# Kernel optimization log

Measured on AMD Instinct MI355X. Metric: run time of the kernel, lower is better.

Reference implementation:

```python
import jax, jax.numpy as jnp
import numpy as np
import math

B, P, D_MODEL, H = 4, 900, 512, 8
NSHOT = 1
SIGMA = 5.0


def setup_inputs() -> dict:
    key = jax.random.key(0)
    ks = jax.random.split(key, 9)
    d, h = D_MODEL, H
    return {
        "query": jax.random.normal(ks[0], (B, P, d), jnp.float32),
        "key_t": jax.random.normal(ks[1], (NSHOT * B, P, d), jnp.float32),
        "value": jax.random.uniform(ks[2], (B, NSHOT * P), dtype=jnp.float32),
        "Wq": jax.random.normal(ks[3], (d, d), jnp.float32) * 0.02,
        "bq": jnp.zeros((d,), jnp.float32),
        "Wk": jax.random.normal(ks[4], (d, d), jnp.float32) * 0.02,
        "bk": jnp.zeros((d,), jnp.float32),
        "conv1_w": jax.random.normal(ks[5], (4 * h, h, 3, 3), jnp.float32) * 0.05,
        "conv1_b": jnp.zeros((4 * h,), jnp.float32),
        "conv2_w": jax.random.normal(ks[6], (h, 4 * h, 3, 3), jnp.float32) * 0.05,
        "conv2_b": jnp.zeros((h,), jnp.float32),
        "nshot": NSHOT,
    }


def _apply_gaussian_kernel(corr, sigma=SIGMA):
    # corr: [Bn, head, HW, W] with HW == W and W a perfect square
    Bn, head, HW, W = corr.shape
    BH = Bn * head
    side = int(round(math.sqrt(W)))
    c = corr.reshape(BH, HW, side, side)
    idx = jnp.argmax(c, axis=1)                                  # [BH, side, side]
    idx_y = (idx // side).astype(jnp.float32)[:, None, None, :, :]
    idx_x = (idx % side).astype(jnp.float32)[:, None, None, :, :]
    xs = jnp.linspace(-1.0, 1.0, side).reshape(1, 1, side, 1, 1)
    ys = jnp.linspace(-1.0, 1.0, side).reshape(1, side, 1, 1, 1)
    # NOTE: original code compares linspace coords to raw integer argmax coords
    gauss = jnp.exp(-((xs - idx_x) ** 2 + (ys - idx_y) ** 2) / (2.0 * sigma ** 2))
    gauss = gauss.reshape(BH, HW, side, side)                    # [BH, h0*w0, h1, w1]
    return (gauss * c).reshape(Bn, head, HW, W)


def reference(query, key_t, value, Wq, bq, Wk, bk, conv1_w, conv1_b, conv2_w, conv2_b, nshot):
    h = conv2_w.shape[0]
    d_model = Wq.shape[0]
    dk = d_model // h
    b, p, _ = query.shape
    n = int(nshot)

    q = (query @ Wq.T + bq).reshape(b, p, h, dk).transpose(0, 2, 1, 3)          # [b,h,p,dk]
    k = (key_t @ Wk.T + bk).reshape(n, b, p, h, dk)
    k = k.transpose(1, 3, 0, 2, 4).reshape(b, h, n * p, dk)                     # [b,h,np,dk]

    scores = jnp.einsum('bhpc,bhqc->bhpq', q, k)                                 # [b,h,p,n*p]

    # gaussian modulation: 'b head h (n w) -> (b n) head h w'
    s = scores.reshape(b, h, p, n, p).transpose(0, 3, 1, 2, 4).reshape(b * n, h, p, p)
    s = _apply_gaussian_kernel(s)
    scores = s.reshape(b, n, h, p, p).transpose(0, 2, 3, 1, 4).reshape(b, h, p, n * p)

    scores = scores / math.sqrt(dk)
    attn = jax.nn.softmax(scores, axis=-1)                                       # [b,h,p,np]

    def conv(x, w, bias):
        y = jax.lax.conv_general_dilated(x, w, (1, 1), 'SAME',
                                         dimension_numbers=('NCHW', 'OIHW', 'NCHW'))
        return jax.nn.relu(y + bias[None, :, None, None])

    attn = conv(attn, conv1_w, conv1_b)
    attn = conv(attn, conv2_w, conv2_b)

    x = jnp.einsum('bhpq,bq->bhp', attn, value)[..., None]                        # [b,h,p,1]
    return jnp.mean(x, axis=1)                                                    # [b,p,1]
```

## Files before the change

kernel.cpp:

```cpp
#include <hip/hip_runtime.h>

#define NB 4
#define NP 900
#define ND 512
#define NH 8
#define NDK 64
#define NROWS (NB*NP)
#define SSZ (NP*NP)
#define NBH (NB*NH)
#define SIDE 30

typedef unsigned short ushort_t;
typedef unsigned char uchar_t;
typedef unsigned long long u64_t;
typedef __attribute__((ext_vector_type(8)))  _Float16 h8v;
typedef __attribute__((ext_vector_type(4)))  float  f4v;
typedef __attribute__((ext_vector_type(16))) float  f16v;

__device__ __forceinline__ ushort_t f2h(float f) {
    union { _Float16 h; ushort_t u; } c; c.h = (_Float16)f; return c.u;
}
__device__ __forceinline__ float h2f(ushort_t u) {
    union { _Float16 h; ushort_t u; } c; c.u = u; return (float)c.h;
}
__device__ __forceinline__ unsigned int fenc(float v) {
    unsigned int b = __float_as_uint(v);
    return (b & 0x80000000u) ? ~b : (b | 0x80000000u);
}

__global__ __launch_bounds__(256) void proj_kernel(
    const float* __restrict__ query, const float* __restrict__ key_t,
    const float* __restrict__ Wq, const float* __restrict__ bq,
    const float* __restrict__ Wk, const float* __restrict__ bk,
    float* __restrict__ Qo, float* __restrict__ Ko, u64_t* __restrict__ amax)
{
    const float *X, *W, *bias;
    float* O;
    if (blockIdx.z == 0) { X = query; W = Wq; bias = bq; O = Qo; }
    else                 { X = key_t; W = Wk; bias = bk; O = Ko; }

    if (blockIdx.z == 0) {
        const int t = (blockIdx.y * 57 + blockIdx.x) * 256 + threadIdx.x;
        if (t < NBH * NP) amax[t] = 0ull;
    }

    __shared__ __align__(16) float As[16][68];
    __shared__ __align__(16) float Bs[16][68];

    const int i0 = blockIdx.x * 64;
    const int h  = blockIdx.y;
    const int j0 = h * 64;
    const int tid = threadIdx.x;
    const int tx = tid & 15, ty = tid >> 4;

    float acc[4][4] = {};

    for (int k0 = 0; k0 < ND; k0 += 16) {
        const int r  = tid >> 2;
        const int kk = (tid & 3) * 4;
        float4 av = make_float4(0.f, 0.f, 0.f, 0.f);
        const int gi = i0 + r;
        if (gi < NROWS) av = *(const float4*)(X + (size_t)gi * ND + k0 + kk);
        As[kk+0][r] = av.x; As[kk+1][r] = av.y; As[kk+2][r] = av.z; As[kk+3][r] = av.w;
        const float4 bv = *(const float4*)(W + (size_t)(j0 + r) * ND + k0 + kk);
        Bs[kk+0][r] = bv.x; Bs[kk+1][r] = bv.y; Bs[kk+2][r] = bv.z; Bs[kk+3][r] = bv.w;
        __syncthreads();
        #pragma unroll
        for (int k = 0; k < 16; ++k) {
            const float4 a4 = *(const float4*)&As[k][ty*4];
            const float4 b4 = *(const float4*)&Bs[k][tx*4];
            const float aa[4] = {a4.x, a4.y, a4.z, a4.w};
            const float bb[4] = {b4.x, b4.y, b4.z, b4.w};
            #pragma unroll
            for (int ii = 0; ii < 4; ++ii)
                #pragma unroll
                for (int jj = 0; jj < 4; ++jj)
                    acc[ii][jj] = fmaf(aa[ii], bb[jj], acc[ii][jj]);
        }
        __syncthreads();
    }

    #pragma unroll
    for (int ii = 0; ii < 4; ++ii) {
        const int gi = i0 + ty*4 + ii;
        if (gi >= NROWS) continue;
        const int b = gi / NP, p = gi - b * NP;
        float4 o;
        o.x = acc[ii][0] + bias[j0 + tx*4 + 0];
        o.y = acc[ii][1] + bias[j0 + tx*4 + 1];
        o.z = acc[ii][2] + bias[j0 + tx*4 + 2];
        o.w = acc[ii][3] + bias[j0 + tx*4 + 3];
        *(float4*)(O + ((size_t)(b*NH + h)*NP + p)*NDK + tx*4) = o;
    }
}

__global__ __launch_bounds__(256, 2) void scores_kernel(
    const float* __restrict__ Q, const float* __restrict__ K, ushort_t* __restrict__ Sh,
    u64_t* __restrict__ amax)
{
    __shared__ __align__(16) ushort_t Qs[128][128];
    __shared__ __align__(16) ushort_t Ks[128][128];
    __shared__ u64_t amax_s[128];

    const int lin = blockIdx.x;
    const int swz = (lin & 7) * 256 + (lin >> 3);
    const int bh  = swz >> 6;
    const int p0  = ((swz >> 3) & 7) * 128;
    const int q0  = (swz & 7) * 128;

    const float* Qb = Q + (size_t)bh * NP * NDK;
    const float* Kb = K + (size_t)bh * NP * NDK;
    const int tid  = threadIdx.x;
    const int lane = tid & 63;
    const int w    = tid >> 6;

    if (tid < 128) amax_s[tid] = 0ull;

    #pragma unroll
    for (int i = 0; i < 8; ++i) {
        const int idx = tid + i * 256;
        const int r = idx >> 4, c4 = idx & 15;
        float4 qv = make_float4(0.f,0.f,0.f,0.f);
        float4 kv = make_float4(0.f,0.f,0.f,0.f);
        if (p0 + r < NP) qv = *(const float4*)(Qb + (size_t)(p0 + r) * NDK + c4*4);
        if (q0 + r < NP) kv = *(const float4*)(Kb + (size_t)(q0 + r) * NDK + c4*4);
        const int ch  = (c4 >> 1) ^ (r & 7);
        const int off = (c4 & 1) * 8;
        const float qf[4] = {qv.x, qv.y, qv.z, qv.w};
        const float kf[4] = {kv.x, kv.y, kv.z, kv.w};
        ushort_t qh[4], ql[4], kh[4], kl[4];
        #pragma unroll
        for (int j = 0; j < 4; ++j) {
            qh[j] = f2h(qf[j]); ql[j] = f2h(qf[j] - h2f(qh[j]));
            kh[j] = f2h(kf[j]); kl[j] = f2h(kf[j] - h2f(kh[j]));
        }
        char* qrow = (char*)&Qs[r][0];
        char* krow = (char*)&Ks[r][0];
        uint2 u;
        u.x = (unsigned)qh[0] | ((unsigned)qh[1] << 16);
        u.y = (unsigned)qh[2] | ((unsigned)qh[3] << 16);
        *(uint2*)(qrow + ch*16 + off) = u;
        u.x = (unsigned)ql[0] | ((unsigned)ql[1] << 16);
        u.y = (unsigned)ql[2] | ((unsigned)ql[3] << 16);
        *(uint2*)(qrow + (ch + 8)*16 + off) = u;
        u.x = (unsigned)kh[0] | ((unsigned)kh[1] << 16);
        u.y = (unsigned)kh[2] | ((unsigned)kh[3] << 16);
        *(uint2*)(krow + ch*16 + off) = u;
        u.x = (unsigned)kl[0] | ((unsigned)kl[1] << 16);
        u.y = (unsigned)kl[2] | ((unsigned)kl[3] << 16);
        *(uint2*)(krow + (ch + 8)*16 + off) = u;
    }
    __syncthreads();

    const int ln = lane & 31;
    const int lh = lane >> 5;
    const int wr = (w >> 1) * 64;
    const int wc = (w & 1) * 64;

    auto ldQ = [&](int row, int ch) -> h8v {
        return *(const h8v*)((const char*)&Qs[row][0] + ((ch ^ (row & 7)) << 4));
    };
    auto ldK = [&](int row, int ch) -> h8v {
        return *(const h8v*)((const char*)&Ks[row][0] + ((ch ^ (row & 7)) << 4));
    };

    f16v acc[2][2] = {};

    #pragma unroll
    for (int ks = 0; ks < 4; ++ks) {
        const int chH = ks*2 + lh;
        h8v ah[2], al[2], bhv[2], blv[2];
        #pragma unroll
        for (int t = 0; t < 2; ++t) {
            const int row = wr + t*32 + ln;
            const int col = wc + t*32 + ln;
            ah[t]  = ldQ(row, chH);
            al[t]  = ldQ(row, chH + 8);
            bhv[t] = ldK(col, chH);
            blv[t] = ldK(col, chH + 8);
        }
        #pragma unroll
        for (int rb = 0; rb < 2; ++rb)
            #pragma unroll
            for (int cb = 0; cb < 2; ++cb) {
                acc[rb][cb] = __builtin_amdgcn_mfma_f32_32x32x16_f16(ah[rb], bhv[cb], acc[rb][cb], 0, 0, 0);
                acc[rb][cb] = __builtin_amdgcn_mfma_f32_32x32x16_f16(ah[rb], blv[cb], acc[rb][cb], 0, 0, 0);
                acc[rb][cb] = __builtin_amdgcn_mfma_f32_32x32x16_f16(al[rb], bhv[cb], acc[rb][cb], 0, 0, 0);
            }
    }

    ushort_t* Sb = Sh + (size_t)bh * SSZ;
    #pragma unroll
    for (int rb = 0; rb < 2; ++rb) {
        #pragma unroll
        for (int cb = 0; cb < 2; ++cb) {
            const int lq = wc + cb*32 + ln;
            const int gq = q0 + lq;
            if (gq < NP) {
                u64_t key = 0ull;
                #pragma unroll
                for (int r = 0; r < 16; ++r) {
                    const int gp = p0 + wr + rb*32 + ((r & 3) + 8*(r >> 2) + 4*lh);
                    if (gp < NP) {
                        const float v = acc[rb][cb][r];
                        Sb[(size_t)gp * NP + gq] = f2h(v);
                        const u64_t kk = ((u64_t)fenc(v) << 32) | (unsigned)(899 - gp);
                        key = key > kk ? key : kk;
                    }
                }
                atomicMax(&amax_s[lq], key);
            }
        }
    }
    __syncthreads();
    if (tid < 128 && q0 + tid < NP)
        atomicMax(&amax[(size_t)bh * NP + q0 + tid], amax_s[tid]);
}

__global__ __launch_bounds__(256) void decode_kernel(
    const u64_t* __restrict__ amax, uchar_t* __restrict__ gidx)
{
    const int t = blockIdx.x * 256 + threadIdx.x;
    if (t >= NBH * NP) return;
    const int idx = 899 - (int)(unsigned)(amax[t] & 0xFFFFFFFFull);
    gidx[2*t]   = (uchar_t)(idx % SIDE);
    gidx[2*t+1] = (uchar_t)(idx / SIDE);
}

__global__ __launch_bounds__(256) void modulate_softmax_kernel(
    const ushort_t* __restrict__ S, const uchar_t* __restrict__ gidx, ushort_t* __restrict__ S2,
    float* __restrict__ out)
{
    __shared__ __align__(16) ushort_t ob[NP][NH];
    __shared__ float TX[SIDE], TY[SIDE];

    const int p = blockIdx.x;
    const int b = blockIdx.y;
    const int tid = threadIdx.x;
    const int lane = tid & 63;
    const int w = tid >> 6;

    if (p == 0)
        for (int q = tid; q < NP; q += 256) out[(size_t)b*NP + q] = 0.f;

    const float ax = -1.f + (2.f/29.f) * (float)(p % SIDE);
    const float ay = -1.f + (2.f/29.f) * (float)(p / SIDE);

    if (tid < SIDE) {
        const float d = ax - (float)tid;
        TX[tid] = __expf(-d*d * 0.02f);
    } else if (tid >= 64 && tid < 64 + SIDE) {
        const int j = tid - 64;
        const float d = ay - (float)j;
        TY[j] = __expf(-d*d * 0.02f);
    }
    __syncthreads();

    #pragma unroll 1
    for (int hh = 0; hh < 2; ++hh) {
        const int h = w + hh*4;
        const ushort_t* row = S + (size_t)(b*NH + h)*SSZ + (size_t)p*NP;
        const uchar_t* gp = gidx + (size_t)(b*NH + h)*NP*2;

        float rv[16];
        float lmax = -3.4e38f;
        #pragma unroll
        for (int i = 0; i < 8; ++i) {
            const int q2 = 2*lane + 128*i;
            float v0 = -3.4e38f, v1 = -3.4e38f;
            if (q2 < NP) {
                const unsigned u = *(const unsigned*)(row + q2);
                const uchar4 g4 = *(const uchar4*)(gp + 2*q2);
                v0 = h2f((ushort_t)(u & 0xFFFFu)) * TX[g4.x] * TY[g4.y] * 0.125f;
                v1 = h2f((ushort_t)(u >> 16))     * TX[g4.z] * TY[g4.w] * 0.125f;
            }
            rv[2*i]   = v0;
            rv[2*i+1] = v1;
            lmax = fmaxf(lmax, fmaxf(v0, v1));
        }
        #pragma unroll
        for (int off = 32; off > 0; off >>= 1)
            lmax = fmaxf(lmax, __shfl_xor(lmax, off, 64));

        float lsum = 0.f;
        #pragma unroll
        for (int i = 0; i < 16; ++i) {
            const int q = 2*lane + 128*(i >> 1) + (i & 1);
            const float e = (q < NP) ? __expf(rv[i] - lmax) : 0.f;
            rv[i] = e;
            lsum += e;
        }
        #pragma unroll
        for (int off = 32; off > 0; off >>= 1)
            lsum += __shfl_xor(lsum, off, 64);
        const float inv = 1.f / lsum;

        #pragma unroll
        for (int i = 0; i < 8; ++i) {
            const int q2 = 2*lane + 128*i;
            if (q2 < NP) {
                ob[q2][h]   = f2h(rv[2*i]   * inv);
                ob[q2+1][h] = f2h(rv[2*i+1] * inv);
            }
        }
    }
    __syncthreads();
    for (int q = tid; q < NP; q += 256)
        *(uint4*)(S2 + (((size_t)b*NP + p)*NP + q)*NH) = *(const uint4*)&ob[q][0];
}

__global__ void prep_weights_kernel(
    const float* __restrict__ c1w, const float* __restrict__ c2w,
    ushort_t* __restrict__ w1b, ushort_t* __restrict__ w2b)
{
    const int tid = threadIdx.x;
    for (int i = tid; i < 5*64; i += 256) {
        const int c = i >> 6, l = i & 63;
        const int oc = l & 31, hf = l >> 5;
        #pragma unroll
        for (int j = 0; j < 8; ++j) {
            float wv;
            if (c < 4)      wv = c1w[(oc*8 + j)*9 + (2*c + hf)];
            else            wv = hf ? 0.f : c1w[(oc*8 + j)*9 + 8];
            w1b[(i)*8 + j] = f2h(wv);
        }
    }
    for (int i = tid; i < 9*64; i += 256) {
        const int t = i >> 6, l = i & 63;
        const int n = l & 15, qd = l >> 4;
        #pragma unroll
        for (int j = 0; j < 8; ++j) {
            const int k = qd*8 + j;
            const float wv = (n < 8) ? c2w[(n*32 + k)*9 + t] : 0.f;
            w2b[(i)*8 + j] = f2h(wv);
        }
    }
}

__global__ __launch_bounds__(256, 4) void conv_mfma_kernel(
    const ushort_t* __restrict__ S2, const ushort_t* __restrict__ w1b,
    const ushort_t* __restrict__ w2b,
    const float* __restrict__ b1, const float* __restrict__ b2,
    const float* __restrict__ value, float* __restrict__ out)
{
    __shared__ __align__(16) ushort_t a_s[4][13][34][8];
    __shared__ __align__(16) ushort_t c1row[4][34][40];

    const int tid  = threadIdx.x;
    const int lane = tid & 63;
    const int w    = tid >> 6;
    const int b    = blockIdx.z;
    const int gx0  = blockIdx.x * 30;
    const int gy0w = blockIdx.y * 36 + w * 9;

    c1row[w][32 + (lane >> 5)][lane & 31] = 0;

    for (int i = lane; i < 13*34; i += 64) {
        const int ai = i / 34, xi = i - ai*34;
        const int gp = gy0w - 2 + ai, gq = gx0 - 2 + xi;
        uint4 v = make_uint4(0u,0u,0u,0u);
        if ((unsigned)gp < (unsigned)NP && (unsigned)gq < (unsigned)NP)
            v = *(const uint4*)(S2 + (((size_t)b*NP + gp)*NP + gq)*NH);
        *(uint4*)&a_s[w][ai][xi][0] = v;
    }

    h8v w1f[5], w2f[9];
    #pragma unroll
    for (int c = 0; c < 5; ++c) w1f[c] = *(const h8v*)(w1b + ((size_t)c*64 + lane)*8);
    #pragma unroll
    for (int t = 0; t < 9; ++t) w2f[t] = *(const h8v*)(w2b + ((size_t)t*64 + lane)*8);

    const float b1v = b1[lane & 31];
    const float b2v = ((lane & 15) < 8) ? b2[lane & 15] : 0.f;

    const int m    = lane & 31;
    const int half = lane >> 5;
    const int m16  = lane & 15;
    const int qd   = lane >> 4;

    float vseg[2][4];
    #pragma unroll
    for (int g = 0; g < 2; ++g)
        #pragma unroll
        for (int r = 0; r < 4; ++r) {
            const int ql = g*16 + qd*4 + r;
            vseg[g][r] = (ql < 30) ? value[b*NP + gx0 + ql] : 0.f;
        }

    auto lda = [&](int y, int x) -> h8v {
        return *(const h8v*)&a_s[w][y][x][0];
    };

    f4v o0[3] = {}, o1[3] = {};

    #pragma unroll
    for (int yc = 0; yc < 11; ++yc) {
        {
            const bool rowok = (unsigned)(gy0w - 1 + yc) < (unsigned)NP;
            const h8v A0 = lda(yc,        m + half);
            const h8v A1 = lda(yc + half, half ? m : (m + 2));
            const h8v A2 = lda(yc + 1,    m + 1 + half);
            const h8v A3 = lda(yc + 2,    m + half);
            const h8v A4 = lda(yc + 2,    m + 2);
            f16v acc = {};
            acc = __builtin_amdgcn_mfma_f32_32x32x16_f16(A0, w1f[0], acc, 0, 0, 0);
            acc = __builtin_amdgcn_mfma_f32_32x32x16_f16(A1, w1f[1], acc, 0, 0, 0);
            acc = __builtin_amdgcn_mfma_f32_32x32x16_f16(A2, w1f[2], acc, 0, 0, 0);
            acc = __builtin_amdgcn_mfma_f32_32x32x16_f16(A3, w1f[3], acc, 0, 0, 0);
            acc = __builtin_amdgcn_mfma_f32_32x32x16_f16(A4, w1f[4], acc, 0, 0, 0);
            #pragma unroll
            for (int r = 0; r < 16; ++r) {
                const int x_l = (r & 3) + 8*(r >> 2) + 4*half;
                float f = fmaxf(acc[r] + b1v, 0.f);
                const bool ok = rowok && ((unsigned)(gx0 - 1 + x_l) < (unsigned)NP);
                f = ok ? f : 0.f;
                c1row[w][x_l][lane & 31] = f2h(f);
            }
        }
        asm volatile("s_waitcnt lgkmcnt(0)" ::: "memory");

        #pragma unroll
        for (int dx = 0; dx < 3; ++dx) {
            const int x0 = m16 + dx, x1 = 16 + m16 + dx;
            const h8v a0 = *(const h8v*)&c1row[w][x0][qd*8];
            const h8v a1 = *(const h8v*)&c1row[w][x1][qd*8];
            #pragma unroll
            for (int dy = 0; dy < 3; ++dy) {
                const int yo = yc - dy;
                if (yo < 0 || yo > 8) continue;
                const int sl = yo % 3;
                o0[sl] = __builtin_amdgcn_mfma_f32_16x16x32_f16(a0, w2f[dy*3+dx], o0[sl], 0, 0, 0);
                o1[sl] = __builtin_amdgcn_mfma_f32_16x16x32_f16(a1, w2f[dy*3+dx], o1[sl], 0, 0, 0);
            }
        }

        if (yc >= 2) {
            const int yo = yc - 2;
            const int sl = yo % 3;
            float s = 0.f;
            const bool ocok = (lane & 15) < 8;
            #pragma unroll
            for (int r = 0; r < 4; ++r) {
                const float f0 = fmaxf(o0[sl][r] + b2v, 0.f);
                const float f1 = fmaxf(o1[sl][r] + b2v, 0.f);
                s += ocok ? f0 * vseg[0][r] : 0.f;
                s += ocok ? f1 * vseg[1][r] : 0.f;
            }
            #pragma unroll
            for (int off = 32; off > 0; off >>= 1)
                s += __shfl_down(s, off, 64);
            if (lane == 0)
                atomicAdd(out + (size_t)b*NP + (gy0w + yo), s * 0.125f);
            o0[sl] = (f4v){0.f,0.f,0.f,0.f};
            o1[sl] = (f4v){0.f,0.f,0.f,0.f};
        }
    }
}

extern "C" void kernel_launch(void* const* d_in, const int* in_sizes, int n_in,
                              void* d_out, int out_size, void* d_ws, size_t ws_size,
                              hipStream_t stream)
{
    const float* query = (const float*)d_in[0];
    const float* key_t = (const float*)d_in[1];
    const float* value = (const float*)d_in[2];
    const float* Wq    = (const float*)d_in[3];
    const float* bq    = (const float*)d_in[4];
    const float* Wk    = (const float*)d_in[5];
    const float* bk    = (const float*)d_in[6];
    const float* c1w   = (const float*)d_in[7];
    const float* c1b   = (const float*)d_in[8];
    const float* c2w   = (const float*)d_in[9];
    const float* c2b   = (const float*)d_in[10];
    float* out = (float*)d_out;

    float*    Q    = (float*)d_ws;
    float*    K    = Q + (size_t)NBH*NP*NDK;
    u64_t*    amax = (u64_t*)(K + (size_t)NBH*NP*NDK);
    uchar_t*  gidx = (uchar_t*)(amax + (size_t)NBH*NP);
    ushort_t* Sh   = (ushort_t*)(gidx + (size_t)NBH*NP*2 + 256);
    ushort_t* S2   = Sh + (size_t)NBH*SSZ;
    ushort_t* w1b  = S2 + (size_t)NB*NP*NP*NH;
    ushort_t* w2b  = w1b + 5*64*8;

    prep_weights_kernel<<<dim3(1), 256, 0, stream>>>(c1w, c2w, w1b, w2b);
    proj_kernel<<<dim3(57, 8, 2), 256, 0, stream>>>(query, key_t, Wq, bq, Wk, bk, Q, K, amax);
    scores_kernel<<<dim3(2048), 256, 0, stream>>>(Q, K, Sh, amax);
    decode_kernel<<<dim3(113), 256, 0, stream>>>(amax, gidx);
    modulate_softmax_kernel<<<dim3(900, 4), 256, 0, stream>>>(Sh, gidx, S2, out);
    conv_mfma_kernel<<<dim3(30, 25, 4), 256, 0, stream>>>(S2, w1b, w2b, c1b, c2b, value, out);
}
```

Baseline: 279.9 us.

## Move Q/K projection GEMM onto split-fp16 MFMA and fold conv biases into accumulators

The projection kernel switches from a scalar FP32 FMA tile to 32x32x16 fp16 MFMA. Inputs and weights are split into hi/lo halves and three products are summed to keep near-FP32 accuracy, with a larger 64x128 tile and fewer column blocks. The split-and-swizzle LDS store is factored into a shared helper that the scores kernel also uses. In the conv kernel, the biases now seed the accumulators instead of being added afterwards, and the output-channel lane mask is dropped. Dropping the mask assumes the padded channels contribute zero; the added cost is extra MFMA work and LDS traffic for the split operands.

```diff
diff --git a/kernel.cpp b/kernel.cpp
--- a/kernel.cpp
+++ b/kernel.cpp
@@ -28,12 +28,34 @@
     return (b & 0x80000000u) ? ~b : (b | 0x80000000u);
 }
 
-__global__ __launch_bounds__(256) void proj_kernel(
+__device__ __forceinline__ void split_store(char* rowp, int r, int c4, float4 v) {
+    const int ch  = (c4 >> 1) ^ (r & 7);
+    const int off = (c4 & 1) * 8;
+    const float f[4] = {v.x, v.y, v.z, v.w};
+    ushort_t hi[4], lo[4];
+    #pragma unroll
+    for (int j = 0; j < 4; ++j) {
+        hi[j] = f2h(f[j]);
+        lo[j] = f2h(f[j] - h2f(hi[j]));
+    }
+    uint2 u;
+    u.x = (unsigned)hi[0] | ((unsigned)hi[1] << 16);
+    u.y = (unsigned)hi[2] | ((unsigned)hi[3] << 16);
+    *(uint2*)(rowp + ch*16 + off) = u;
+    u.x = (unsigned)lo[0] | ((unsigned)lo[1] << 16);
+    u.y = (unsigned)lo[2] | ((unsigned)lo[3] << 16);
+    *(uint2*)(rowp + (ch + 8)*16 + off) = u;
+}
+
+__global__ __launch_bounds__(256, 3) void proj_kernel(
     const float* __restrict__ query, const float* __restrict__ key_t,
     const float* __restrict__ Wq, const float* __restrict__ bq,
     const float* __restrict__ Wk, const float* __restrict__ bk,
     float* __restrict__ Qo, float* __restrict__ Ko, u64_t* __restrict__ amax)
 {
+    __shared__ __align__(16) ushort_t As[64][128];
+    __shared__ __align__(16) ushort_t Bs[128][128];
+
     const float *X, *W, *bias;
     float* O;
     if (blockIdx.z == 0) { X = query; W = Wq; bias = bq; O = Qo; }
@@ -44,53 +66,79 @@
         if (t < NBH * NP) amax[t] = 0ull;
     }
 
-    __shared__ __align__(16) float As[16][68];
-    __shared__ __align__(16) float Bs[16][68];
-
-    const int i0 = blockIdx.x * 64;
-    const int h  = blockIdx.y;
-    const int j0 = h * 64;
-    const int tid = threadIdx.x;
-    const int tx = tid & 15, ty = tid >> 4;
-
-    float acc[4][4] = {};
-
-    for (int k0 = 0; k0 < ND; k0 += 16) {
-        const int r  = tid >> 2;
-        const int kk = (tid & 3) * 4;
-        float4 av = make_float4(0.f, 0.f, 0.f, 0.f);
-        const int gi = i0 + r;
-        if (gi < NROWS) av = *(const float4*)(X + (size_t)gi * ND + k0 + kk);
-        As[kk+0][r] = av.x; As[kk+1][r] = av.y; As[kk+2][r] = av.z; As[kk+3][r] = av.w;
-        const float4 bv = *(const float4*)(W + (size_t)(j0 + r) * ND + k0 + kk);
-        Bs[kk+0][r] = bv.x; Bs[kk+1][r] = bv.y; Bs[kk+2][r] = bv.z; Bs[kk+3][r] = bv.w;
+    const int m0 = blockIdx.x * 64;
+    const int n0 = blockIdx.y * 128;
+    const int tid  = threadIdx.x;
+    const int lane = tid & 63;
+    const int w    = tid >> 6;
+    const int ln = lane & 31, lh = lane >> 5;
+    const int wr = (w >> 1) * 32;
+    const int wc = (w & 1) * 64;
+
+    f16v acc[2];
+    #pragma unroll
+    for (int cb = 0; cb < 2; ++cb) {
+        const float bv = bias[n0 + wc + cb*32 + ln];
+        #pragma unroll
+        for (int r = 0; r < 16; ++r) acc[cb][r] = bv;
+    }
+
+    auto ldA = [&](int row, int ch) -> h8v {
+        return *(const h8v*)((const char*)&As[row][0] + ((ch ^ (row & 7)) << 4));
+    };
+    auto ldB = [&](int row, int ch) -> h8v {
+        return *(const h8v*)((const char*)&Bs[row][0] + ((ch ^ (row & 7)) << 4));
+    };
+
+    for (int kt = 0; kt < 8; ++kt) {
+        const int kb = kt * 64;
+        #pragma unroll
+        for (int i = 0; i < 4; ++i) {
+            const int idx = tid + i * 256;
+            const int r = idx >> 4, c4 = idx & 15;
+            float4 v = make_float4(0.f, 0.f, 0.f, 0.f);
+            if (m0 + r < NROWS) v = *(const float4*)(X + (size_t)(m0 + r) * ND + kb + c4*4);
+            split_store((char*)&As[r][0], r, c4, v);
+        }
+        #pragma unroll
+        for (int i = 0; i < 8; ++i) {
+            const int idx = tid + i * 256;
+            const int r = idx >> 4, c4 = idx & 15;
+            const float4 v = *(const float4*)(W + (size_t)(n0 + r) * ND + kb + c4*4);
+            split_store((char*)&Bs[r][0], r, c4, v);
+        }
         __syncthreads();
-        #pragma unroll
-        for (int k = 0; k < 16; ++k) {
-            const float4 a4 = *(const float4*)&As[k][ty*4];
-            const float4 b4 = *(const float4*)&Bs[k][tx*4];
-            const float aa[4] = {a4.x, a4.y, a4.z, a4.w};
-            const float bb[4] = {b4.x, b4.y, b4.z, b4.w};
-            #pragma unroll
-            for (int ii = 0; ii < 4; ++ii)
-                #pragma unroll
-                for (int jj = 0; jj < 4; ++jj)
-                    acc[ii][jj] = fmaf(aa[ii], bb[jj], acc[ii][jj]);
+
+        #pragma unroll
+        for (int ks = 0; ks < 4; ++ks) {
+            const int chH = ks*2 + lh;
+            const h8v a_h = ldA(wr + ln, chH);
+            const h8v a_l = ldA(wr + ln, chH + 8);
+            #pragma unroll
+            for (int cb = 0; cb < 2; ++cb) {
+                const int col = wc + cb*32 + ln;
+                const h8v b_h = ldB(col, chH);
+                const h8v b_l = ldB(col, chH + 8);
+                acc[cb] = __builtin_amdgcn_mfma_f32_32x32x16_f16(a_h, b_h, acc[cb], 0, 0, 0);
+                acc[cb] = __builtin_amdgcn_mfma_f32_32x32x16_f16(a_h, b_l, acc[cb], 0, 0, 0);
+                acc[cb] = __builtin_amdgcn_mfma_f32_32x32x16_f16(a_l, b_h, acc[cb], 0, 0, 0);
+            }
         }
         __syncthreads();
     }
 
     #pragma unroll
-    for (int ii = 0; ii < 4; ++ii) {
-        const int gi = i0 + ty*4 + ii;
-        if (gi >= NROWS) continue;
-        const int b = gi / NP, p = gi - b * NP;
-        float4 o;
-        o.x = acc[ii][0] + bias[j0 + tx*4 + 0];
-        o.y = acc[ii][1] + bias[j0 + tx*4 + 1];
-        o.z = acc[ii][2] + bias[j0 + tx*4 + 2];
-        o.w = acc[ii][3] + bias[j0 + tx*4 + 3];
-        *(float4*)(O + ((size_t)(b*NH + h)*NP + p)*NDK + tx*4) = o;
+    for (int cb = 0; cb < 2; ++cb) {
+        const int col = n0 + wc + cb*32 + ln;
+        const int h = col >> 6, dk = col & 63;
+        #pragma unroll
+        for (int r = 0; r < 16; ++r) {
+            const int gi = m0 + wr + ((r & 3) + 8*(r >> 2) + 4*lh);
+            if (gi < NROWS) {
+                const int bb = gi / NP, p = gi - bb * NP;
+                O[((size_t)(bb*NH + h)*NP + p)*NDK + dk] = acc[cb][r];
+            }
+        }
     }
 }
 
@@ -124,31 +172,8 @@
         float4 kv = make_float4(0.f,0.f,0.f,0.f);
         if (p0 + r < NP) qv = *(const float4*)(Qb + (size_t)(p0 + r) * NDK + c4*4);
         if (q0 + r < NP) kv = *(const float4*)(Kb + (size_t)(q0 + r) * NDK + c4*4);
-        const int ch  = (c4 >> 1) ^ (r & 7);
-        const int off = (c4 & 1) * 8;
-        const float qf[4] = {qv.x, qv.y, qv.z, qv.w};
-        const float kf[4] = {kv.x, kv.y, kv.z, kv.w};
-        ushort_t qh[4], ql[4], kh[4], kl[4];
-        #pragma unroll
-        for (int j = 0; j < 4; ++j) {
-            qh[j] = f2h(qf[j]); ql[j] = f2h(qf[j] - h2f(qh[j]));
-            kh[j] = f2h(kf[j]); kl[j] = f2h(kf[j] - h2f(kh[j]));
-        }
-        char* qrow = (char*)&Qs[r][0];
-        char* krow = (char*)&Ks[r][0];
-        uint2 u;
-        u.x = (unsigned)qh[0] | ((unsigned)qh[1] << 16);
-        u.y = (unsigned)qh[2] | ((unsigned)qh[3] << 16);
-        *(uint2*)(qrow + ch*16 + off) = u;
-        u.x = (unsigned)ql[0] | ((unsigned)ql[1] << 16);
-        u.y = (unsigned)ql[2] | ((unsigned)ql[3] << 16);
-        *(uint2*)(qrow + (ch + 8)*16 + off) = u;
-        u.x = (unsigned)kh[0] | ((unsigned)kh[1] << 16);
-        u.y = (unsigned)kh[2] | ((unsigned)kh[3] << 16);
-        *(uint2*)(krow + ch*16 + off) = u;
-        u.x = (unsigned)kl[0] | ((unsigned)kl[1] << 16);
-        u.y = (unsigned)kl[2] | ((unsigned)kl[3] << 16);
-        *(uint2*)(krow + (ch + 8)*16 + off) = u;
+        split_store((char*)&Qs[r][0], r, c4, qv);
+        split_store((char*)&Ks[r][0], r, c4, kv);
     }
     __syncthreads();
 
@@ -391,7 +416,12 @@
         return *(const h8v*)&a_s[w][y][x][0];
     };
 
-    f4v o0[3] = {}, o1[3] = {};
+    f4v o0[3], o1[3];
+    #pragma unroll
+    for (int sl = 0; sl < 3; ++sl) {
+        o0[sl] = (f4v){b2v, b2v, b2v, b2v};
+        o1[sl] = (f4v){b2v, b2v, b2v, b2v};
+    }
 
     #pragma unroll
     for (int yc = 0; yc < 11; ++yc) {
@@ -402,7 +432,9 @@
             const h8v A2 = lda(yc + 1,    m + 1 + half);
             const h8v A3 = lda(yc + 2,    m + half);
             const h8v A4 = lda(yc + 2,    m + 2);
-            f16v acc = {};
+            f16v acc;
+            #pragma unroll
+            for (int r = 0; r < 16; ++r) acc[r] = b1v;
             acc = __builtin_amdgcn_mfma_f32_32x32x16_f16(A0, w1f[0], acc, 0, 0, 0);
             acc = __builtin_amdgcn_mfma_f32_32x32x16_f16(A1, w1f[1], acc, 0, 0, 0);
             acc = __builtin_amdgcn_mfma_f32_32x32x16_f16(A2, w1f[2], acc, 0, 0, 0);
@@ -411,7 +443,7 @@
             #pragma unroll
             for (int r = 0; r < 16; ++r) {
                 const int x_l = (r & 3) + 8*(r >> 2) + 4*half;
-                float f = fmaxf(acc[r] + b1v, 0.f);
+                float f = fmaxf(acc[r], 0.f);
                 const bool ok = rowok && ((unsigned)(gx0 - 1 + x_l) < (unsigned)NP);
                 f = ok ? f : 0.f;
                 c1row[w][x_l][lane & 31] = f2h(f);
@@ -438,21 +470,19 @@
             const int yo = yc - 2;
             const int sl = yo % 3;
             float s = 0.f;
-            const bool ocok = (lane & 15) < 8;
             #pragma unroll
             for (int r = 0; r < 4; ++r) {
-                const float f0 = fmaxf(o0[sl][r] + b2v, 0.f);
-                const float f1 = fmaxf(o1[sl][r] + b2v, 0.f);
-                s += ocok ? f0 * vseg[0][r] : 0.f;
-                s += ocok ? f1 * vseg[1][r] : 0.f;
+                const float f0 = fmaxf(o0[sl][r], 0.f);
+                const float f1 = fmaxf(o1[sl][r], 0.f);
+                s += f0 * vseg[0][r] + f1 * vseg[1][r];
             }
             #pragma unroll
             for (int off = 32; off > 0; off >>= 1)
                 s += __shfl_down(s, off, 64);
             if (lane == 0)
                 atomicAdd(out + (size_t)b*NP + (gy0w + yo), s * 0.125f);
-            o0[sl] = (f4v){0.f,0.f,0.f,0.f};
-            o1[sl] = (f4v){0.f,0.f,0.f,0.f};
+            o0[sl] = (f4v){b2v, b2v, b2v, b2v};
+            o1[sl] = (f4v){b2v, b2v, b2v, b2v};
         }
     }
 }
@@ -484,7 +514,7 @@
     ushort_t* w2b  = w1b + 5*64*8;
 
     prep_weights_kernel<<<dim3(1), 256, 0, stream>>>(c1w, c2w, w1b, w2b);
-    proj_kernel<<<dim3(57, 8, 2), 256, 0, stream>>>(query, key_t, Wq, bq, Wk, bk, Q, K, amax);
+    proj_kernel<<<dim3(57, 4, 2), 256, 0, stream>>>(query, key_t, Wq, bq, Wk, bk, Q, K, amax);
     scores_kernel<<<dim3(2048), 256, 0, stream>>>(Q, K, Sh, amax);
     decode_kernel<<<dim3(113), 256, 0, stream>>>(amax, gidx);
     modulate_softmax_kernel<<<dim3(900, 4), 256, 0, stream>>>(Sh, gidx, S2, out);
```

New measurement: 275.2 us. No clear change (-1.7%).
